# Kernel tuning notes

Hardware: AMD Instinct MI355X
Metric: run time of the kernel (lower is better)

Reference implementation:

```python
import jax, jax.numpy as jnp
import numpy as np

DIM, D_INNER, D_STATE, DT_RANK, D_CONV = 1024, 2048, 16, 64, 4
BATCH, SEQ = 2, 1024

def setup_inputs() -> dict:
    key = jax.random.key(0)
    ks = jax.random.split(key, 9)
    s = 0.02
    A = jnp.tile(jnp.arange(1, D_STATE + 1, dtype=jnp.float32), (D_INNER, 1))
    return {
        "x": jax.random.normal(ks[0], (BATCH, SEQ, DIM), jnp.float32),
        "in_proj_w": jax.random.normal(ks[1], (DIM, 2 * D_INNER), jnp.float32) * s,
        "conv_w": jax.random.normal(ks[2], (D_INNER, 1, D_CONV), jnp.float32) * 0.2,
        "conv_b": jax.random.normal(ks[3], (D_INNER,), jnp.float32) * 0.1,
        "x_proj_w": jax.random.normal(ks[4], (D_INNER, DT_RANK + 2 * D_STATE), jnp.float32) * s,
        "dt_proj_w": jax.random.normal(ks[5], (DT_RANK, D_INNER), jnp.float32) * s,
        "dt_proj_b": jax.random.normal(ks[6], (D_INNER,), jnp.float32) * 0.1,
        "A_log": jnp.log(A),
        "D_param": jnp.ones((D_INNER,), jnp.float32),
        "out_proj_w": jax.random.normal(ks[7], (D_INNER, DIM), jnp.float32) * s,
    }

def _silu(v):
    return v * jax.nn.sigmoid(v)

def _ssm_forward(x, in_proj_w, conv_w, conv_b, x_proj_w, dt_proj_w, dt_proj_b, A_log, D_param, out_proj_w):
    b, l, _ = x.shape
    d_inner, d_conv = conv_w.shape[0], conv_w.shape[2]
    dt_rank, n = dt_proj_w.shape[0], A_log.shape[1]
    # input projection and split into conv branch / gate branch
    x_and_res = x @ in_proj_w                      # (b, l, 2*d_inner)
    xp, res = x_and_res[..., :d_inner], x_and_res[..., d_inner:]
    # causal depthwise conv (torch pads d_conv-1 both sides then slices [:l])
    h = jax.lax.conv_general_dilated(
        xp.transpose(0, 2, 1), conv_w,
        window_strides=(1,), padding=[(d_conv - 1, 0)],
        dimension_numbers=("NCH", "OIH", "NCH"),
        feature_group_count=d_inner,
    ) + conv_b[None, :, None]                      # (b, d_inner, l)
    h = _silu(h.transpose(0, 2, 1))                # (b, l, d_inner)
    # input-dependent SSM parameters
    A = -jnp.exp(A_log)                            # (d_inner, n)
    x_dbl = h @ x_proj_w                           # (b, l, dt_rank + 2n)
    dlt, Bm, Cm = (x_dbl[..., :dt_rank],
                   x_dbl[..., dt_rank:dt_rank + n],
                   x_dbl[..., dt_rank + n:])
    delta = jax.nn.softplus(dlt @ dt_proj_w + dt_proj_b)   # (b, l, d_inner)
    # discretization
    deltaA = jnp.exp(jnp.einsum("bld,dn->bldn", delta, A))             # (b,l,d,n)
    deltaB_u = (delta * h)[..., None] * Bm[:, :, None, :]              # (b,l,d,n)
    # sequential selective scan over time via lax.scan
    def step(state, t):
        dA_t, dBu_t, c_t = t
        state = dA_t * state + dBu_t               # (b, d, n)
        y_t = jnp.einsum("bdn,bn->bd", state, c_t)
        return state, y_t
    init = jnp.zeros((b, d_inner, n), h.dtype)
    _, ys = jax.lax.scan(step, init,
                         (deltaA.transpose(1, 0, 2, 3),
                          deltaB_u.transpose(1, 0, 2, 3),
                          Cm.transpose(1, 0, 2)))
    y = ys.transpose(1, 0, 2) + h * D_param        # (b, l, d_inner)
    y = y * _silu(res)
    return y @ out_proj_w                          # (b, l, dim)

def reference(x, in_proj_w, conv_w, conv_b, x_proj_w, dt_proj_w, dt_proj_b, A_log, D_param, out_proj_w):
    return _ssm_forward(x, in_proj_w, conv_w, conv_b, x_proj_w, dt_proj_w, dt_proj_b, A_log, D_param, out_proj_w)
```

## Files before the change

kernel.cpp:

```cpp
#include <hip/hip_runtime.h>
#include <hip/hip_bf16.h>

#define DIM     1024
#define DINNER  2048
#define NSTATE  16
#define DTRANK  64
#define DCONV   4
#define BATCH   2
#define SEQ     1024
#define BL      (BATCH*SEQ)
#define XDBLW   96
#define NCHUNK  32
#define TCHUNK  32
#define KSLICE  16
#define G4SK    4
#define LOG2E   1.44269504088896f
#define LN2     0.69314718055995f

typedef __attribute__((ext_vector_type(4))) float  f32x4;
typedef __attribute__((ext_vector_type(8))) short  bf16x8;
typedef unsigned short ushort_t;

__device__ __forceinline__ ushort_t f2bf(float f) {
    union { float f; unsigned int u; } v; v.f = f;
    unsigned int lsb = (v.u >> 16) & 1u;
    v.u += 0x7fffu + lsb;
    return (ushort_t)(v.u >> 16);
}
__device__ __forceinline__ float bf2f(ushort_t h) {
    union { unsigned u; float f; } v; v.u = ((unsigned)h) << 16; return v.f;
}
__device__ __forceinline__ float hexp2(float x) { return __builtin_amdgcn_exp2f(x); }
__device__ __forceinline__ float hlog2(float x) { return __builtin_amdgcn_logf(x); }
__device__ __forceinline__ float hrcp(float x)  { return __builtin_amdgcn_rcpf(x); }
__device__ __forceinline__ float softplus_fast(float x) {
    float e = hexp2(-fabsf(x) * LOG2E);
    return fmaxf(x, 0.f) + LN2 * hlog2(1.f + e);
}
__device__ __forceinline__ float sigmoid_fast(float x) {
    return hrcp(1.f + hexp2(-x * LOG2E));
}

typedef __attribute__((address_space(1))) unsigned int gu32_t;
typedef __attribute__((address_space(3))) unsigned int lu32_t;
__device__ __forceinline__ void gload_lds16(const ushort_t* g, ushort_t* l) {
    __builtin_amdgcn_global_load_lds((const gu32_t*)(const void*)g,
                                     (lu32_t*)(void*)l, 16, 0, 0);
}

__global__ __launch_bounds__(256) void prep_fused(
    const float* __restrict__ Win,  ushort_t* __restrict__ WtIn,
    const float* __restrict__ Wout, ushort_t* __restrict__ WtOut,
    const float* __restrict__ Wxp,  ushort_t* __restrict__ WtXp,
    const float* __restrict__ x,    ushort_t* __restrict__ xb)
{
    __shared__ float tile[32][33];
    const int tid = threadIdx.x;
    const int tx = tid & 31, ty = tid >> 5;
    const int bid = blockIdx.x;

    const float* src; ushort_t* dst; int R, C, bx, by;
    if (bid < 4096)      { src = Win;  dst = WtIn;  R = 1024; C = 4096; int j = bid;        bx = j % 128; by = j / 128; }
    else if (bid < 6144) { src = Wout; dst = WtOut; R = 2048; C = 1024; int j = bid - 4096; bx = j % 32;  by = j / 32; }
    else if (bid < 6336) { src = Wxp;  dst = WtXp;  R = 2048; C = 96;   int j = bid - 6144; bx = j % 3;   by = j / 3; }
    else {
        int i = ((bid - 6336) * 256 + tid) * 4;
        f32x4 v = *(const f32x4*)(x + i);
        ushort_t r0 = f2bf(v[0]), r1 = f2bf(v[1]), r2 = f2bf(v[2]), r3 = f2bf(v[3]);
        *(uint2*)(xb + i) = make_uint2((unsigned)r0 | ((unsigned)r1 << 16),
                                       (unsigned)r2 | ((unsigned)r3 << 16));
        return;
    }

    const int r0 = by * 32, c0 = bx * 32;
    #pragma unroll
    for (int i = 0; i < 4; ++i)
        tile[ty + i * 8][tx] = src[(size_t)(r0 + ty + i * 8) * C + c0 + tx];
    __syncthreads();
    #pragma unroll
    for (int i = 0; i < 4; ++i)
        dst[(size_t)(c0 + ty + i * 8) * R + r0 + tx] = f2bf(tile[tx][ty + i * 8]);
}

__global__ __launch_bounds__(256) void gemm_lds(
    const ushort_t* __restrict__ A,  int lda,
    const ushort_t* __restrict__ Bt, int ldb,
    int K,
    float* __restrict__ Cf, ushort_t* __restrict__ Cb, int ldc)
{
    __shared__ ushort_t As[128 * 32];
    __shared__ ushort_t Bs[128 * 32];

    const int tid  = threadIdx.x;
    const int m0   = blockIdx.y * 128;
    const int n0   = blockIdx.x * 128;
    const int wid  = tid >> 6;
    const int lane = tid & 63;
    const int wm   = (wid >> 1) * 64;
    const int wn   = (wid & 1) * 64;
    const int lr   = lane & 15;
    const int lk   = (lane >> 4) * 8;

    const int c0 = wid * 64 + lane;
    const int c1 = 256 + c0;
    const int r0 = c0 >> 2, f0 = (c0 & 3) * 8;
    const int r1 = c1 >> 2, f1 = (c1 & 3) * 8;
    ushort_t* lA0 = &As[(wid * 64) * 8];
    ushort_t* lA1 = &As[(256 + wid * 64) * 8];
    ushort_t* lB0 = &Bs[(wid * 64) * 8];
    ushort_t* lB1 = &Bs[(256 + wid * 64) * 8];

    f32x4 acc[4][4];
    #pragma unroll
    for (int m = 0; m < 4; ++m)
        #pragma unroll
        for (int n = 0; n < 4; ++n)
            acc[m][n] = (f32x4){0.f, 0.f, 0.f, 0.f};

    for (int k0 = 0; k0 < K; k0 += 32) {
        gload_lds16(A  + (size_t)(m0 + r0) * lda + k0 + f0, lA0);
        gload_lds16(A  + (size_t)(m0 + r1) * lda + k0 + f1, lA1);
        gload_lds16(Bt + (size_t)(n0 + r0) * ldb + k0 + f0, lB0);
        gload_lds16(Bt + (size_t)(n0 + r1) * ldb + k0 + f1, lB1);
        __syncthreads();

        bf16x8 af[4], bfr[4];
        #pragma unroll
        for (int m = 0; m < 4; ++m)
            af[m] = *(const bf16x8*)(&As[(wm + m * 16 + lr) * 32 + lk]);
        #pragma unroll
        for (int n = 0; n < 4; ++n)
            bfr[n] = *(const bf16x8*)(&Bs[(wn + n * 16 + lr) * 32 + lk]);

        #pragma unroll
        for (int m = 0; m < 4; ++m)
            #pragma unroll
            for (int n = 0; n < 4; ++n)
                acc[m][n] = __builtin_amdgcn_mfma_f32_16x16x32_bf16(af[m], bfr[n], acc[m][n], 0, 0, 0);
        __syncthreads();
    }

    const int rbase = (lane >> 4) * 4;
    #pragma unroll
    for (int m = 0; m < 4; ++m) {
        #pragma unroll
        for (int n = 0; n < 4; ++n) {
            int col = n0 + wn + n * 16 + lr;
            #pragma unroll
            for (int r = 0; r < 4; ++r) {
                int row = m0 + wm + m * 16 + rbase + r;
                float v = acc[m][n][r];
                if (Cf) Cf[(size_t)row * ldc + col] = v;
                if (Cb) Cb[(size_t)row * ldc + col] = f2bf(v);
            }
        }
    }
}

__global__ __launch_bounds__(256) void gemm_lds_sk(
    const ushort_t* __restrict__ A,  int lda,
    const ushort_t* __restrict__ Bt, int ldb,
    int klen,
    float* __restrict__ Part, int ldc, int mn)
{
    __shared__ ushort_t As[128 * 32];
    __shared__ ushort_t Bs[128 * 32];

    const int tid  = threadIdx.x;
    const int m0   = blockIdx.y * 128;
    const int n0   = blockIdx.x * 128;
    const int kb   = blockIdx.z * klen;
    float* Cf = Part + (size_t)blockIdx.z * mn;

    const int wid  = tid >> 6;
    const int lane = tid & 63;
    const int wm   = (wid >> 1) * 64;
    const int wn   = (wid & 1) * 64;
    const int lr   = lane & 15;
    const int lk   = (lane >> 4) * 8;

    const int c0 = wid * 64 + lane;
    const int c1 = 256 + c0;
    const int r0 = c0 >> 2, f0 = (c0 & 3) * 8;
    const int r1 = c1 >> 2, f1 = (c1 & 3) * 8;
    ushort_t* lA0 = &As[(wid * 64) * 8];
    ushort_t* lA1 = &As[(256 + wid * 64) * 8];
    ushort_t* lB0 = &Bs[(wid * 64) * 8];
    ushort_t* lB1 = &Bs[(256 + wid * 64) * 8];

    f32x4 acc[4][4];
    #pragma unroll
    for (int m = 0; m < 4; ++m)
        #pragma unroll
        for (int n = 0; n < 4; ++n)
            acc[m][n] = (f32x4){0.f, 0.f, 0.f, 0.f};

    for (int k0 = kb; k0 < kb + klen; k0 += 32) {
        gload_lds16(A  + (size_t)(m0 + r0) * lda + k0 + f0, lA0);
        gload_lds16(A  + (size_t)(m0 + r1) * lda + k0 + f1, lA1);
        gload_lds16(Bt + (size_t)(n0 + r0) * ldb + k0 + f0, lB0);
        gload_lds16(Bt + (size_t)(n0 + r1) * ldb + k0 + f1, lB1);
        __syncthreads();

        bf16x8 af[4], bfr[4];
        #pragma unroll
        for (int m = 0; m < 4; ++m)
            af[m] = *(const bf16x8*)(&As[(wm + m * 16 + lr) * 32 + lk]);
        #pragma unroll
        for (int n = 0; n < 4; ++n)
            bfr[n] = *(const bf16x8*)(&Bs[(wn + n * 16 + lr) * 32 + lk]);

        #pragma unroll
        for (int m = 0; m < 4; ++m)
            #pragma unroll
            for (int n = 0; n < 4; ++n)
                acc[m][n] = __builtin_amdgcn_mfma_f32_16x16x32_bf16(af[m], bfr[n], acc[m][n], 0, 0, 0);
        __syncthreads();
    }

    const int rbase = (lane >> 4) * 4;
    #pragma unroll
    for (int m = 0; m < 4; ++m) {
        #pragma unroll
        for (int n = 0; n < 4; ++n) {
            int col = n0 + wn + n * 16 + lr;
            #pragma unroll
            for (int r = 0; r < 4; ++r) {
                int row = m0 + wm + m * 16 + rbase + r;
                Cf[(size_t)row * ldc + col] = acc[m][n][r];
            }
        }
    }
}

__global__ __launch_bounds__(256) void g4_reduce(
    const float* __restrict__ Part, float* __restrict__ out)
{
    int i = (blockIdx.x * 256 + threadIdx.x) * 4;
    const size_t mn = (size_t)BL * DIM;
    f32x4 s = *(const f32x4*)(Part + i);
    #pragma unroll
    for (int z = 1; z < G4SK; ++z)
        s += *(const f32x4*)(Part + z * mn + i);
    *(f32x4*)(out + i) = s;
}

__global__ __launch_bounds__(256) void gemm_n96_splitk(
    const ushort_t* __restrict__ A,
    const ushort_t* __restrict__ Bt,
    float* __restrict__ Ppart)
{
    __shared__ ushort_t As[128 * 40];
    __shared__ ushort_t Bs[96 * 40];

    const int tid   = threadIdx.x;
    const int ks    = blockIdx.x;
    const int m0    = blockIdx.y * 128;
    const int kbase = ks * (DINNER / KSLICE);
    const int wid   = tid >> 6;
    const int lane  = tid & 63;
    const int wm    = wid * 32;
    const int lr    = lane & 15;
    const int lk    = (lane >> 4) * 8;

    f32x4 acc[2][6];
    #pragma unroll
    for (int m = 0; m < 2; ++m)
        #pragma unroll
        for (int n = 0; n < 6; ++n)
            acc[m][n] = (f32x4){0.f, 0.f, 0.f, 0.f};

    for (int k0 = kbase; k0 < kbase + DINNER / KSLICE; k0 += 32) {
        #pragma unroll
        for (int c = 0; c < 2; ++c) {
            int cid = tid + c * 256;
            int row = cid >> 2, ck = (cid & 3) * 8;
            *(uint4*)(&As[row * 40 + ck]) =
                *(const uint4*)(A + (size_t)(m0 + row) * DINNER + k0 + ck);
        }
        {
            int row = tid >> 2, ck = (tid & 3) * 8;
            *(uint4*)(&Bs[row * 40 + ck]) =
                *(const uint4*)(Bt + (size_t)row * DINNER + k0 + ck);
            if (tid < 128) {
                int cid = 256 + tid;
                int row2 = cid >> 2, ck2 = (cid & 3) * 8;
                *(uint4*)(&Bs[row2 * 40 + ck2]) =
                    *(const uint4*)(Bt + (size_t)row2 * DINNER + k0 + ck2);
            }
        }
        __syncthreads();

        bf16x8 af[2], bfr[6];
        #pragma unroll
        for (int m = 0; m < 2; ++m)
            af[m] = *(const bf16x8*)(&As[(wm + m * 16 + lr) * 40 + lk]);
        #pragma unroll
        for (int n = 0; n < 6; ++n)
            bfr[n] = *(const bf16x8*)(&Bs[(n * 16 + lr) * 40 + lk]);

        #pragma unroll
        for (int m = 0; m < 2; ++m)
            #pragma unroll
            for (int n = 0; n < 6; ++n)
                acc[m][n] = __builtin_amdgcn_mfma_f32_16x16x32_bf16(af[m], bfr[n], acc[m][n], 0, 0, 0);
        __syncthreads();
    }

    const int rbase = (lane >> 4) * 4;
    #pragma unroll
    for (int m = 0; m < 2; ++m) {
        #pragma unroll
        for (int n = 0; n < 6; ++n) {
            int col = n * 16 + lr;
            #pragma unroll
            for (int r = 0; r < 4; ++r) {
                int row = m0 + wm + m * 16 + rbase + r;
                Ppart[((size_t)ks * BL + row) * XDBLW + col] = acc[m][n][r];
            }
        }
    }
}

__global__ __launch_bounds__(256) void g2_reduce(
    const float* __restrict__ Ppart, float* __restrict__ xdbl)
{
    int idx = blockIdx.x * 256 + threadIdx.x;
    int row = idx / 24, cg = (idx % 24) * 4;
    f32x4 s = (f32x4){0.f, 0.f, 0.f, 0.f};
    #pragma unroll
    for (int ks = 0; ks < KSLICE; ++ks)
        s += *(const f32x4*)(Ppart + ((size_t)ks * BL + row) * XDBLW + cg);
    *(f32x4*)(xdbl + (size_t)row * XDBLW + cg) = s;
}

__global__ __launch_bounds__(256, 4) void delta_v6(
    const float* __restrict__ xdbl,
    const float* __restrict__ Wdt,
    const float* __restrict__ dtb,
    ushort_t* __restrict__ delta_bf)
{
    __shared__ float WS[64][256];
    __shared__ float dS[32][64];
    const int tid  = threadIdx.x;
    const int d0   = (blockIdx.x & 7) * 256;
    const int row0 = (blockIdx.x >> 3) * 32;

    #pragma unroll
    for (int i = 0; i < 16; ++i) {
        int c = i * 256 + tid;
        int k = c >> 6, co = (c & 63) * 4;
        *(f32x4*)&WS[k][co] = *(const f32x4*)(Wdt + (size_t)k * DINNER + d0 + co);
    }
    #pragma unroll
    for (int i = 0; i < 2; ++i) {
        int c = i * 256 + tid;
        int r = c >> 4, co = (c & 15) * 4;
        *(f32x4*)&dS[r][co] = *(const f32x4*)(xdbl + (size_t)(row0 + r) * XDBLW + co);
    }
    __syncthreads();

    const int w    = tid >> 6;
    const int lane = tid & 63;
    const int dd   = lane * 4;

    f32x4 acc[8];
    {
        f32x4 bb = *(const f32x4*)(dtb + d0 + dd);
        #pragma unroll
        for (int r = 0; r < 8; ++r) acc[r] = bb;
    }

    for (int kq = 0; kq < 16; ++kq) {
        f32x4 dv[8];
        #pragma unroll
        for (int r = 0; r < 8; ++r)
            dv[r] = *(const f32x4*)&dS[w * 8 + r][kq * 4];
        #pragma unroll
        for (int kk = 0; kk < 4; ++kk) {
            f32x4 wv = *(const f32x4*)&WS[kq * 4 + kk][dd];
            #pragma unroll
            for (int r = 0; r < 8; ++r) {
                float dk = dv[r][kk];
                acc[r][0] = fmaf(dk, wv[0], acc[r][0]);
                acc[r][1] = fmaf(dk, wv[1], acc[r][1]);
                acc[r][2] = fmaf(dk, wv[2], acc[r][2]);
                acc[r][3] = fmaf(dk, wv[3], acc[r][3]);
            }
        }
    }

    #pragma unroll
    for (int r = 0; r < 8; ++r) {
        const size_t rowb = (size_t)(row0 + w * 8 + r) * DINNER + d0;
        f32x4 v = acc[r];
        ushort_t o[4];
        #pragma unroll
        for (int j = 0; j < 4; ++j)
            o[j] = f2bf(softplus_fast(v[j]));
        *(uint2*)(delta_bf + rowb + dd) = make_uint2(
            (unsigned)o[0] | ((unsigned)o[1] << 16), (unsigned)o[2] | ((unsigned)o[3] << 16));
    }
}

__global__ __launch_bounds__(256) void conv_silu(
    const ushort_t* __restrict__ xrb,
    const float* __restrict__ convw,
    const float* __restrict__ convb,
    ushort_t* __restrict__ hb)
{
    const int d  = blockIdx.x * 256 + threadIdx.x;
    const int bt = blockIdx.y;
    const int t  = bt & (SEQ - 1);

    float acc = convb[d];
    #pragma unroll
    for (int j = 0; j < DCONV; ++j) {
        int tt = t + j - (DCONV - 1);
        if (tt >= 0)
            acc += convw[d * DCONV + j] * bf2f(xrb[(size_t)(bt + j - (DCONV - 1)) * 4096 + d]);
    }
    float h = acc * sigmoid_fast(acc);
    hb[(size_t)bt * DINNER + d] = f2bf(h);
}

__global__ __launch_bounds__(256) void scan_p1(
    const ushort_t* __restrict__ delta_bf,
    const ushort_t* __restrict__ hb,
    const float* __restrict__ xdbl,
    const float* __restrict__ Alog,
    float* __restrict__ Pbuf,
    float* __restrict__ Sbuf)
{
    const int d  = (blockIdx.x & 7) * 256 + threadIdx.x;
    const int bc = blockIdx.x >> 3;
    const int b  = bc >> 5;
    const int c  = bc & (NCHUNK - 1);
    const int t0 = c * TCHUNK;

    float A[NSTATE];
    #pragma unroll
    for (int q = 0; q < 4; ++q) {
        f32x4 al = *(const f32x4*)(Alog + (size_t)d * NSTATE + q * 4);
        #pragma unroll
        for (int j = 0; j < 4; ++j)
            A[q * 4 + j] = -hexp2(al[j] * LOG2E) * LOG2E;
    }

    float s[NSTATE], pp[NSTATE];
    #pragma unroll
    for (int n = 0; n < NSTATE; ++n) { s[n] = 0.f; pp[n] = 1.f; }

    for (int tt = 0; tt < TCHUNK; ++tt) {
        const size_t row = (size_t)(b * SEQ + t0 + tt);
        float dl = bf2f(delta_bf[row * DINNER + d]);
        float hv = bf2f(hb[row * DINNER + d]);
        float dlh = dl * hv;
        float Bv[NSTATE];
        #pragma unroll
        for (int q = 0; q < 4; ++q) {
            f32x4 bv = *(const f32x4*)(xdbl + row * XDBLW + DTRANK + q * 4);
            #pragma unroll
            for (int j = 0; j < 4; ++j) Bv[q * 4 + j] = bv[j];
        }
        #pragma unroll
        for (int n = 0; n < NSTATE; ++n) {
            float a = hexp2(dl * A[n]);
            s[n]  = fmaf(a, s[n], dlh * Bv[n]);
            pp[n] *= a;
        }
    }

    const size_t o = (((size_t)b * NCHUNK + c) * DINNER + d) * NSTATE;
    #pragma unroll
    for (int q = 0; q < 4; ++q) {
        *(f32x4*)(Sbuf + o + q * 4) = (f32x4){s[q*4+0], s[q*4+1], s[q*4+2], s[q*4+3]};
        *(f32x4*)(Pbuf + o + q * 4) = (f32x4){pp[q*4+0], pp[q*4+1], pp[q*4+2], pp[q*4+3]};
    }
}

__global__ __launch_bounds__(256) void scan_p2(
    const float* __restrict__ Pbuf, float* __restrict__ Sbuf)
{
    const int tid = blockIdx.x * 256 + threadIdx.x;
    const int n = tid & 15;
    const int d = (tid >> 4) & (DINNER - 1);
    const int b = tid >> 15;
    const size_t stride = (size_t)DINNER * NSTATE;
    size_t idx = ((size_t)b * NCHUNK * DINNER + d) * NSTATE + n;
    float cin = 0.f;
    for (int c = 0; c < NCHUNK; ++c, idx += stride) {
        float S = Sbuf[idx];
        float P = Pbuf[idx];
        Sbuf[idx] = cin;
        cin = fmaf(P, cin, S);
    }
}

__global__ __launch_bounds__(256) void scan_p3(
    const ushort_t* __restrict__ delta_bf,
    const ushort_t* __restrict__ hb,
    const float* __restrict__ xdbl,
    const ushort_t* __restrict__ xrb,
    const float* __restrict__ Alog,
    const float* __restrict__ Dp,
    const float* __restrict__ Sbuf,
    ushort_t* __restrict__ yb)
{
    const int d  = (blockIdx.x & 7) * 256 + threadIdx.x;
    const int bc = blockIdx.x >> 3;
    const int b  = bc >> 5;
    const int c  = bc & (NCHUNK - 1);
    const int t0 = c * TCHUNK;

    float A[NSTATE];
    #pragma unroll
    for (int q = 0; q < 4; ++q) {
        f32x4 al = *(const f32x4*)(Alog + (size_t)d * NSTATE + q * 4);
        #pragma unroll
        for (int j = 0; j < 4; ++j)
            A[q * 4 + j] = -hexp2(al[j] * LOG2E) * LOG2E;
    }
    const float Dd = Dp[d];

    float s[NSTATE];
    const size_t o = (((size_t)b * NCHUNK + c) * DINNER + d) * NSTATE;
    #pragma unroll
    for (int q = 0; q < 4; ++q) {
        f32x4 sv = *(const f32x4*)(Sbuf + o + q * 4);
        #pragma unroll
        for (int j = 0; j < 4; ++j) s[q * 4 + j] = sv[j];
    }

    for (int tt = 0; tt < TCHUNK; ++tt) {
        const size_t row = (size_t)(b * SEQ + t0 + tt);
        float dl = bf2f(delta_bf[row * DINNER + d]);
        float hv = bf2f(hb[row * DINNER + d]);
        float rv = bf2f(xrb[row * 4096 + DINNER + d]);
        float dlh = dl * hv;
        float Bv[NSTATE], Cv[NSTATE];
        #pragma unroll
        for (int q = 0; q < 4; ++q) {
            f32x4 bv = *(const f32x4*)(xdbl + row * XDBLW + DTRANK + q * 4);
            f32x4 cv = *(const f32x4*)(xdbl + row * XDBLW + DTRANK + NSTATE + q * 4);
            #pragma unroll
            for (int j = 0; j < 4; ++j) { Bv[q*4+j] = bv[j]; Cv[q*4+j] = cv[j]; }
        }
        float y = 0.f;
        #pragma unroll
        for (int n = 0; n < NSTATE; ++n) {
            float a = hexp2(dl * A[n]);
            s[n] = fmaf(a, s[n], dlh * Bv[n]);
            y = fmaf(s[n], Cv[n], y);
        }
        y = fmaf(hv, Dd, y);
        y = y * rv * sigmoid_fast(rv);
        yb[row * DINNER + d] = f2bf(y);
    }
}

extern "C" void kernel_launch(void* const* d_in, const int* in_sizes, int n_in,
                              void* d_out, int out_size, void* d_ws, size_t ws_size,
                              hipStream_t stream)
{
    const float* x     = (const float*)d_in[0];
    const float* Win   = (const float*)d_in[1];
    const float* convw = (const float*)d_in[2];
    const float* convb = (const float*)d_in[3];
    const float* Wxp   = (const float*)d_in[4];
    const float* Wdt   = (const float*)d_in[5];
    const float* dtb   = (const float*)d_in[6];
    const float* Alog  = (const float*)d_in[7];
    const float* Dp    = (const float*)d_in[8];
    const float* Wout  = (const float*)d_in[9];
    float* out = (float*)d_out;

    char* base = (char*)d_ws; size_t off = 0;
    auto alloc = [&](size_t bytes) -> char* {
        char* q = base + off;
        off = (off + bytes + 255) & ~(size_t)255;
        return q;
    };
    ushort_t* WtIn   = (ushort_t*)alloc((size_t)4096 * 1024 * 2);
    ushort_t* WtOut  = (ushort_t*)alloc((size_t)1024 * 2048 * 2);
    ushort_t* WtXp   = (ushort_t*)alloc((size_t)96   * 2048 * 2);
    ushort_t* xb     = (ushort_t*)alloc((size_t)BL * DIM * 2);
    ushort_t* xrb    = (ushort_t*)alloc((size_t)BL * 4096 * 2);
    ushort_t* hb     = (ushort_t*)alloc((size_t)BL * DINNER * 2);
    float*    xdbl   = (float*)   alloc((size_t)BL * XDBLW * 4);
    ushort_t* dltbf  = (ushort_t*)alloc((size_t)BL * DINNER * 2);
    ushort_t* yb     = (ushort_t*)alloc((size_t)BL * DINNER * 2);
    float*    Pbuf   = (float*)   alloc((size_t)BATCH * NCHUNK * DINNER * NSTATE * 4);
    float*    Sbuf   = (float*)   alloc((size_t)BATCH * NCHUNK * DINNER * NSTATE * 4);
    float*    Ppart  = (float*)   alloc((size_t)KSLICE * BL * XDBLW * 4);
    float*    G4part = (float*)   alloc((size_t)G4SK * BL * DIM * 4);
    (void)ws_size;

    prep_fused<<<dim3(8384), 256, 0, stream>>>(Win, WtIn, Wout, WtOut, Wxp, WtXp, x, xb);

    gemm_lds<<<dim3(4096/128, BL/128), 256, 0, stream>>>(
        xb, DIM, WtIn, DIM, DIM, nullptr, xrb, 2*DINNER);

    conv_silu<<<dim3(DINNER/256, BL), 256, 0, stream>>>(xrb, convw, convb, hb);

    gemm_n96_splitk<<<dim3(KSLICE, BL/128), 256, 0, stream>>>(hb, WtXp, Ppart);
    g2_reduce<<<dim3(BL * 24 / 256), 256, 0, stream>>>(Ppart, xdbl);

    delta_v6<<<dim3(8 * (BL / 32)), 256, 0, stream>>>(xdbl, Wdt, dtb, dltbf);

    scan_p1<<<dim3(8 * BATCH * NCHUNK), 256, 0, stream>>>(dltbf, hb, xdbl, Alog, Pbuf, Sbuf);
    scan_p2<<<dim3(BATCH * DINNER * NSTATE / 256), 256, 0, stream>>>(Pbuf, Sbuf);
    scan_p3<<<dim3(8 * BATCH * NCHUNK), 256, 0, stream>>>(dltbf, hb, xdbl, xrb, Alog, Dp, Sbuf, yb);

    gemm_lds_sk<<<dim3(DIM/128, BL/128, G4SK), 256, 0, stream>>>(
        yb, DINNER, WtOut, DINNER, DINNER/G4SK, G4part, DIM, BL*DIM);
    g4_reduce<<<dim3(BL*DIM/4/256), 256, 0, stream>>>(G4part, out);
}
```

Before: 159.6 us.

## Double-buffer LDS tiles in bf16 GEMM kernels to overlap loads with MFMA

Both GEMM kernels now keep two LDS buffers for the A and B tiles. The next K-slice is prefetched with direct global-to-LDS loads while MFMAs run on the current slice, and partial vmcnt waits plus raw s_barrier replace the full __syncthreads. This is meant to hide global load latency behind compute. In exchange it doubles LDS use per block, which may lower occupancy, and it depends on hand-written waitcnt correctness.

Result: faster. 154.5 us (-3.2%).

```diff
diff --git a/kernel.cpp b/kernel.cpp
--- a/kernel.cpp
+++ b/kernel.cpp
@@ -88,8 +88,8 @@
     int K,
     float* __restrict__ Cf, ushort_t* __restrict__ Cb, int ldc)
 {
-    __shared__ ushort_t As[128 * 32];
-    __shared__ ushort_t Bs[128 * 32];
+    __shared__ ushort_t As[2][128 * 32];
+    __shared__ ushort_t Bs[2][128 * 32];
 
     const int tid  = threadIdx.x;
     const int m0   = blockIdx.y * 128;
@@ -105,10 +105,8 @@
     const int c1 = 256 + c0;
     const int r0 = c0 >> 2, f0 = (c0 & 3) * 8;
     const int r1 = c1 >> 2, f1 = (c1 & 3) * 8;
-    ushort_t* lA0 = &As[(wid * 64) * 8];
-    ushort_t* lA1 = &As[(256 + wid * 64) * 8];
-    ushort_t* lB0 = &Bs[(wid * 64) * 8];
-    ushort_t* lB1 = &Bs[(256 + wid * 64) * 8];
+    const int lo0 = (wid * 64) * 8;
+    const int lo1 = (256 + wid * 64) * 8;
 
     f32x4 acc[4][4];
     #pragma unroll
@@ -117,27 +115,42 @@
         for (int n = 0; n < 4; ++n)
             acc[m][n] = (f32x4){0.f, 0.f, 0.f, 0.f};
 
-    for (int k0 = 0; k0 < K; k0 += 32) {
-        gload_lds16(A  + (size_t)(m0 + r0) * lda + k0 + f0, lA0);
-        gload_lds16(A  + (size_t)(m0 + r1) * lda + k0 + f1, lA1);
-        gload_lds16(Bt + (size_t)(n0 + r0) * ldb + k0 + f0, lB0);
-        gload_lds16(Bt + (size_t)(n0 + r1) * ldb + k0 + f1, lB1);
-        __syncthreads();
+    const int nk = K >> 5;
+
+    gload_lds16(A  + (size_t)(m0 + r0) * lda + f0, &As[0][lo0]);
+    gload_lds16(A  + (size_t)(m0 + r1) * lda + f1, &As[0][lo1]);
+    gload_lds16(Bt + (size_t)(n0 + r0) * ldb + f0, &Bs[0][lo0]);
+    gload_lds16(Bt + (size_t)(n0 + r1) * ldb + f1, &Bs[0][lo1]);
+
+    for (int k = 0; k < nk; ++k) {
+        const int cur = k & 1;
+        if (k + 1 < nk) {
+            const int k0 = (k + 1) << 5;
+            gload_lds16(A  + (size_t)(m0 + r0) * lda + k0 + f0, &As[cur ^ 1][lo0]);
+            gload_lds16(A  + (size_t)(m0 + r1) * lda + k0 + f1, &As[cur ^ 1][lo1]);
+            gload_lds16(Bt + (size_t)(n0 + r0) * ldb + k0 + f0, &Bs[cur ^ 1][lo0]);
+            gload_lds16(Bt + (size_t)(n0 + r1) * ldb + k0 + f1, &Bs[cur ^ 1][lo1]);
+            asm volatile("s_waitcnt vmcnt(4)" ::: "memory");
+        } else {
+            asm volatile("s_waitcnt vmcnt(0)" ::: "memory");
+        }
+        __builtin_amdgcn_sched_barrier(0);
+        __builtin_amdgcn_s_barrier();
 
         bf16x8 af[4], bfr[4];
         #pragma unroll
         for (int m = 0; m < 4; ++m)
-            af[m] = *(const bf16x8*)(&As[(wm + m * 16 + lr) * 32 + lk]);
+            af[m] = *(const bf16x8*)(&As[cur][(wm + m * 16 + lr) * 32 + lk]);
         #pragma unroll
         for (int n = 0; n < 4; ++n)
-            bfr[n] = *(const bf16x8*)(&Bs[(wn + n * 16 + lr) * 32 + lk]);
+            bfr[n] = *(const bf16x8*)(&Bs[cur][(wn + n * 16 + lr) * 32 + lk]);
 
         #pragma unroll
         for (int m = 0; m < 4; ++m)
             #pragma unroll
             for (int n = 0; n < 4; ++n)
                 acc[m][n] = __builtin_amdgcn_mfma_f32_16x16x32_bf16(af[m], bfr[n], acc[m][n], 0, 0, 0);
-        __syncthreads();
+        __builtin_amdgcn_s_barrier();
     }
 
     const int rbase = (lane >> 4) * 4;
@@ -163,8 +176,8 @@
     int klen,
     float* __restrict__ Part, int ldc, int mn)
 {
-    __shared__ ushort_t As[128 * 32];
-    __shared__ ushort_t Bs[128 * 32];
+    __shared__ ushort_t As[2][128 * 32];
+    __shared__ ushort_t Bs[2][128 * 32];
 
     const int tid  = threadIdx.x;
     const int m0   = blockIdx.y * 128;
@@ -183,10 +196,8 @@
     const int c1 = 256 + c0;
     const int r0 = c0 >> 2, f0 = (c0 & 3) * 8;
     const int r1 = c1 >> 2, f1 = (c1 & 3) * 8;
-    ushort_t* lA0 = &As[(wid * 64) * 8];
-    ushort_t* lA1 = &As[(256 + wid * 64) * 8];
-    ushort_t* lB0 = &Bs[(wid * 64) * 8];
-    ushort_t* lB1 = &Bs[(256 + wid * 64) * 8];
+    const int lo0 = (wid * 64) * 8;
+    const int lo1 = (256 + wid * 64) * 8;
 
     f32x4 acc[4][4];
     #pragma unroll
@@ -195,27 +206,42 @@
         for (int n = 0; n < 4; ++n)
             acc[m][n] = (f32x4){0.f, 0.f, 0.f, 0.f};
 
-    for (int k0 = kb; k0 < kb + klen; k0 += 32) {
-        gload_lds16(A  + (size_t)(m0 + r0) * lda + k0 + f0, lA0);
-        gload_lds16(A  + (size_t)(m0 + r1) * lda + k0 + f1, lA1);
-        gload_lds16(Bt + (size_t)(n0 + r0) * ldb + k0 + f0, lB0);
-        gload_lds16(Bt + (size_t)(n0 + r1) * ldb + k0 + f1, lB1);
-        __syncthreads();
+    const int nk = klen >> 5;
+
+    gload_lds16(A  + (size_t)(m0 + r0) * lda + kb + f0, &As[0][lo0]);
+    gload_lds16(A  + (size_t)(m0 + r1) * lda + kb + f1, &As[0][lo1]);
+    gload_lds16(Bt + (size_t)(n0 + r0) * ldb + kb + f0, &Bs[0][lo0]);
+    gload_lds16(Bt + (size_t)(n0 + r1) * ldb + kb + f1, &Bs[0][lo1]);
+
+    for (int k = 0; k < nk; ++k) {
+        const int cur = k & 1;
+        if (k + 1 < nk) {
+            const int k0 = kb + ((k + 1) << 5);
+            gload_lds16(A  + (size_t)(m0 + r0) * lda + k0 + f0, &As[cur ^ 1][lo0]);
+            gload_lds16(A  + (size_t)(m0 + r1) * lda + k0 + f1, &As[cur ^ 1][lo1]);
+            gload_lds16(Bt + (size_t)(n0 + r0) * ldb + k0 + f0, &Bs[cur ^ 1][lo0]);
+            gload_lds16(Bt + (size_t)(n0 + r1) * ldb + k0 + f1, &Bs[cur ^ 1][lo1]);
+            asm volatile("s_waitcnt vmcnt(4)" ::: "memory");
+        } else {
+            asm volatile("s_waitcnt vmcnt(0)" ::: "memory");
+        }
+        __builtin_amdgcn_sched_barrier(0);
+        __builtin_amdgcn_s_barrier();
 
         bf16x8 af[4], bfr[4];
         #pragma unroll
         for (int m = 0; m < 4; ++m)
-            af[m] = *(const bf16x8*)(&As[(wm + m * 16 + lr) * 32 + lk]);
+            af[m] = *(const bf16x8*)(&As[cur][(wm + m * 16 + lr) * 32 + lk]);
         #pragma unroll
         for (int n = 0; n < 4; ++n)
-            bfr[n] = *(const bf16x8*)(&Bs[(wn + n * 16 + lr) * 32 + lk]);
+            bfr[n] = *(const bf16x8*)(&Bs[cur][(wn + n * 16 + lr) * 32 + lk]);
 
         #pragma unroll
         for (int m = 0; m < 4; ++m)
             #pragma unroll
             for (int n = 0; n < 4; ++n)
                 acc[m][n] = __builtin_amdgcn_mfma_f32_16x16x32_bf16(af[m], bfr[n], acc[m][n], 0, 0, 0);
-        __syncthreads();
+        __builtin_amdgcn_s_barrier();
     }
 
     const int rbase = (lane >> 4) * 4;
```
